# Performance work log

Hardware: AMD Instinct MI355X
Metric: run time of the kernel (lower is better)

The kernel has to match this reference:

```python
import jax, jax.numpy as jnp
import numpy as np
import math

D_MODEL = 1024
N_HEADS = 16
D_HEAD = D_MODEL // N_HEADS
LSR_RANK = 32
B, T = 4, 2048


def setup_inputs() -> dict:
    key = jax.random.key(0)
    ks = jax.random.split(key, 11)
    s = 1.0 / math.sqrt(D_MODEL)
    x = jax.random.normal(ks[0], (B, T, D_MODEL), dtype=jnp.float32)
    Wq = jax.random.uniform(ks[1], (D_MODEL, D_MODEL), minval=-s, maxval=s)
    bq = jax.random.uniform(ks[2], (D_MODEL,), minval=-s, maxval=s)
    Wk = jax.random.uniform(ks[3], (D_MODEL, D_MODEL), minval=-s, maxval=s)
    bk = jax.random.uniform(ks[4], (D_MODEL,), minval=-s, maxval=s)
    Wv = jax.random.uniform(ks[5], (D_MODEL, D_MODEL), minval=-s, maxval=s)
    bv = jax.random.uniform(ks[6], (D_MODEL,), minval=-s, maxval=s)
    Wo = jax.random.uniform(ks[7], (D_MODEL, D_MODEL), minval=-s, maxval=s)
    bo = jax.random.uniform(ks[8], (D_MODEL,), minval=-s, maxval=s)
    Wq_lsr = jax.random.normal(ks[9], (N_HEADS, D_HEAD, LSR_RANK)) / math.sqrt(D_HEAD)
    Wk_lsr = jax.random.normal(ks[10], (N_HEADS, D_HEAD, LSR_RANK)) / math.sqrt(D_HEAD)
    return {"x": x, "Wq": Wq, "bq": bq, "Wk": Wk, "bk": bk,
            "Wv": Wv, "bv": bv, "Wo": Wo, "bo": bo,
            "Wq_lsr": Wq_lsr, "Wk_lsr": Wk_lsr}


def reference(x, Wq, bq, Wk, bk, Wv, bv, Wo, bo, Wq_lsr, Wk_lsr):
    Bq, Tq, _ = x.shape
    # Linear projections (torch Linear: x @ W.T + b), split into heads -> (B,H,T,Dh)
    def split_heads(y):
        return y.reshape(Bq, Tq, N_HEADS, D_HEAD).transpose(0, 2, 1, 3)
    q = split_heads(x @ Wq.T + bq)
    k = split_heads(x @ Wk.T + bk)
    v = split_heads(x @ Wv.T + bv)
    # LSR: project q,k to rank-R per head
    q_lr = jnp.einsum('bhtd,hdr->bhtr', q, Wq_lsr)
    k_lr = jnp.einsum('bhtd,hdr->bhtr', k, Wk_lsr)
    scale = 1.0 / math.sqrt(max(LSR_RANK, 1))
    scores = jnp.einsum('bhir,bhjr->bhij', q_lr, k_lr) * scale  # (B,H,T,T)
    causal_mask = jnp.triu(jnp.ones((Tq, Tq), dtype=bool), k=1)
    scores = jnp.where(causal_mask, jnp.float32(-jnp.inf), scores)
    attn = jax.nn.softmax(scores, axis=-1)
    y = jnp.einsum('bhij,bhjd->bhid', attn, v)  # (B,H,T,Dh)
    y = y.transpose(0, 2, 1, 3).reshape(Bq, Tq, D_MODEL)
    return y @ Wo.T + bo
```

## Files before the change

### kernel.cpp

```cpp
#include <hip/hip_runtime.h>

#define B_  4
#define T_  2048
#define H_  16
#define DM_ 1024
#define DH_ 64
#define RK_ 32

using u16 = unsigned short;
using u32 = unsigned int;
typedef float  floatx4 __attribute__((ext_vector_type(4)));
typedef __bf16 bf16x8  __attribute__((ext_vector_type(8)));
typedef u16    u16x8   __attribute__((ext_vector_type(8)));
typedef u16    u16x4   __attribute__((ext_vector_type(4)));
typedef short  s16x4   __attribute__((ext_vector_type(4)));

#define MFMA16(a,b,c) __builtin_amdgcn_mfma_f32_16x16x32_bf16((a),(b),(c),0,0,0)
#define MFMA1K(a,b,c) __builtin_amdgcn_mfma_f32_16x16x16bf16_1k((a),(b),(c),0,0,0)

__device__ __forceinline__ u16 f2bf(float f) {
  unsigned u = __float_as_uint(f);
  u += 0x7fffu + ((u >> 16) & 1u);
  return (u16)(u >> 16);
}
__device__ __forceinline__ u32 pack_bf(float a, float b) {
  u32 ua = __float_as_uint(a); ua += 0x7fffu + ((ua >> 16) & 1u);
  u32 ub = __float_as_uint(b); ub += 0x7fffu + ((ub >> 16) & 1u);
  return __builtin_amdgcn_perm(ub, ua, 0x07060302u);
}
__device__ __forceinline__ u32 tpack(float a, float b) {
  return __builtin_amdgcn_perm(__float_as_uint(b), __float_as_uint(a), 0x07060302u);
}

__device__ __forceinline__ void async_copy16(const u16* g, const u16* lds_uniform_base) {
  __builtin_amdgcn_global_load_lds(
      (const __attribute__((address_space(1))) unsigned int*)(unsigned long long)g,
      (__attribute__((address_space(3))) unsigned int*)(unsigned int)(unsigned long long)lds_uniform_base,
      16, 0, 0);
}

__global__ __launch_bounds__(256) void cvt_x(const float* __restrict__ s,
                                             u16* __restrict__ d, int n4) {
  int i = blockIdx.x * 256 + threadIdx.x;
  if (i >= n4) return;
  float4 v = reinterpret_cast<const float4*>(s)[i];
  u16x4 o = { f2bf(v.x), f2bf(v.y), f2bf(v.z), f2bf(v.w) };
  reinterpret_cast<u16x4*>(d)[i] = o;
}

__global__ __launch_bounds__(256) void prep_w(const float* __restrict__ Wv,
                                              const float* __restrict__ Wo,
                                              const float* __restrict__ Wq,
                                              const float* __restrict__ bq,
                                              const float* __restrict__ Wql,
                                              const float* __restrict__ Wk,
                                              const float* __restrict__ bk,
                                              const float* __restrict__ Wkl,
                                              u16* __restrict__ Wcat,
                                              float* __restrict__ beffq,
                                              float* __restrict__ beffk) {
  const int tid = threadIdx.x;
  const int bid = blockIdx.x;
  __shared__ float lw[64];
  if (bid < 2048) {
    int i = bid * 256 + tid;
    int reg = i >> 18;
    const float* s = reg ? Wo : Wv;
    int j = i & 262143;
    float4 v = reinterpret_cast<const float4*>(s)[j];
    u16x4 o = { f2bf(v.x), f2bf(v.y), f2bf(v.z), f2bf(v.w) };
    reinterpret_cast<u16x4*>(Wcat)[(reg ? 524288 : 0) + j] = o;
    return;
  }
  const int sel = (bid >= 2560);
  const int hr = bid - (sel ? 2560 : 2048);
  const int h = hr >> 5, r = hr & 31;
  const float* W    = sel ? Wk : Wq;
  const float* bias = sel ? bk : bq;
  const float* lsr  = sel ? Wkl : Wql;
  const float fold  = sel ? 1.0f : 0.25506100790944405f;
  u16*   Weff = Wcat + (sel ? 1572864 : 1048576);
  float* beff = sel ? beffk : beffq;
  if (tid < 64) lw[tid] = lsr[(size_t)(h * 64 + tid) * 32 + r] * fold;
  __syncthreads();
  float a0 = 0.f, a1 = 0.f, a2 = 0.f, a3 = 0.f;
  for (int d = 0; d < 64; d++) {
    float l = lw[d];
    float4 wv = *reinterpret_cast<const float4*>(W + (size_t)(h * 64 + d) * 1024 + tid * 4);
    a0 += l * wv.x; a1 += l * wv.y; a2 += l * wv.z; a3 += l * wv.w;
  }
  u16x4 o = { f2bf(a0), f2bf(a1), f2bf(a2), f2bf(a3) };
  reinterpret_cast<u16x4*>(Weff)[(size_t)hr * 256 + tid] = o;
  if (tid == 0) {
    float s = 0.f;
    for (int d = 0; d < 64; d++) s += lw[d] * bias[h * 64 + d];
    beff[hr] = s;
  }
}

template <int MODE>
__global__ __launch_bounds__(256, 2) void gemm8(const u16* __restrict__ A,
                                                const u16* __restrict__ W,
                                                const float* __restrict__ b0,
                                                const float* __restrict__ b1,
                                                const float* __restrict__ b2,
                                                void* __restrict__ Cv,
                                                u16* __restrict__ qo,
                                                u16* __restrict__ ko,
                                                int ldc) {
  __shared__ __align__(16) u16 Al[2][8192];
  __shared__ __align__(16) u16 Bl[2][8192];
  const int tid  = threadIdx.x;
  const int lane = tid & 63;
  const int w    = tid >> 6;
  const int quad = lane >> 4;
  const int l16  = lane & 15;
  const int wm   = (w >> 1) << 6;
  const int wn   = (w & 1) << 6;

  const int bm = blockIdx.x << 7;
  const int bn = blockIdx.y << 7;

  const int sr = tid >> 3;
  const int sc = ((tid & 7) ^ (sr & 7)) * 8;
  const u16* Ag = A + (size_t)(bm + sr) * 1024 + sc;
  const u16* Wg = W + (size_t)(bn + sr) * 1024 + sc;

  auto stage = [&](int k0, int bsel) {
#pragma unroll
    for (int j = 0; j < 4; j++)
      async_copy16(Ag + (size_t)j * 32768 + k0, &Al[bsel][j * 2048 + w * 512]);
#pragma unroll
    for (int j = 0; j < 4; j++)
      async_copy16(Wg + (size_t)j * 32768 + k0, &Bl[bsel][j * 2048 + w * 512]);
  };

  int aoff[4], boff[4], sl[2];
#pragma unroll
  for (int mi = 0; mi < 4; mi++) aoff[mi] = (wm + mi * 16 + l16) * 64;
#pragma unroll
  for (int ni = 0; ni < 4; ni++) boff[ni] = (wn + ni * 16 + l16) * 64;
  sl[0] = ((0 + quad) ^ (l16 & 7)) * 8;
  sl[1] = ((4 + quad) ^ (l16 & 7)) * 8;

  floatx4 acc[4][4];
#pragma unroll
  for (int i = 0; i < 4; i++)
#pragma unroll
    for (int j = 0; j < 4; j++) acc[i][j] = (floatx4){0.f, 0.f, 0.f, 0.f};

  stage(0, 0);
  asm volatile("s_waitcnt vmcnt(0)" ::: "memory");
  __builtin_amdgcn_s_barrier();
  asm volatile("" ::: "memory");

  for (int i = 0; i < 16; i++) {
    if (i < 15) stage((i + 1) * 64, (i + 1) & 1);
    const u16* Ab = Al[i & 1];
    const u16* Bb = Bl[i & 1];
#pragma unroll
    for (int ks = 0; ks < 2; ks++) {
      bf16x8 af[4], bfr[4];
#pragma unroll
      for (int mi = 0; mi < 4; mi++)
        af[mi] = *reinterpret_cast<const bf16x8*>(Ab + aoff[mi] + sl[ks]);
#pragma unroll
      for (int ni = 0; ni < 4; ni++)
        bfr[ni] = *reinterpret_cast<const bf16x8*>(Bb + boff[ni] + sl[ks]);
      __builtin_amdgcn_s_setprio(1);
#pragma unroll
      for (int mi = 0; mi < 4; mi++)
#pragma unroll
        for (int ni = 0; ni < 4; ni++)
          acc[mi][ni] = MFMA16(af[mi], bfr[ni], acc[mi][ni]);
      __builtin_amdgcn_s_setprio(0);
    }
    if (i < 15) {
      asm volatile("s_waitcnt vmcnt(0)" ::: "memory");
      __builtin_amdgcn_s_barrier();
      asm volatile("" ::: "memory");
    }
  }

  if (MODE == 1) {
#pragma unroll
    for (int ni = 0; ni < 4; ni++) {
      int col = bn + wn + ni * 16 + l16;
      float bias = b0[col & 1023];
#pragma unroll
      for (int mi = 0; mi < 4; mi++)
#pragma unroll
        for (int r = 0; r < 4; r++) {
          int row = bm + wm + mi * 16 + quad * 4 + r;
          reinterpret_cast<float*>(Cv)[(size_t)row * ldc + col] = acc[mi][ni][r] + bias;
        }
    }
  } else {
    if (bn < 1024) {
#pragma unroll
      for (int ni = 0; ni < 4; ni++) {
        int col = bn + wn + ni * 16 + l16;
        float bias = b0[col];
#pragma unroll
        for (int mi = 0; mi < 4; mi++)
#pragma unroll
          for (int r = 0; r < 4; r++) {
            int row = bm + wm + mi * 16 + quad * 4 + r;
            reinterpret_cast<u16*>(Cv)[(size_t)row * 1024 + col] =
                f2bf(acc[mi][ni][r] + bias);
          }
      }
    } else {
      u16* outp = (bn < 1536) ? qo : ko;
      const float* bp = (bn < 1536) ? b1 : b2;
#pragma unroll
      for (int ni = 0; ni < 4; ni++) {
        int cc = (bn + wn + ni * 16 + l16) & 511;
        float bias = bp[cc];
        int hh = cc >> 5, rk = cc & 31;
#pragma unroll
        for (int mi = 0; mi < 4; mi++)
#pragma unroll
          for (int r = 0; r < 4; r++) {
            int row = bm + wm + mi * 16 + quad * 4 + r;
            size_t addr =
                ((size_t)((row >> 11) * 16 + hh) * 2048 + (row & 2047)) * 32 + rk;
            outp[addr] = f2bf(acc[mi][ni][r] + bias);
          }
      }
    }
  }
}

__global__ __launch_bounds__(256) void vtrans(const u16* __restrict__ V,
                                              u16* __restrict__ vt) {
  const int tb = blockIdx.x;
  const int bh = blockIdx.y;
  const int b = bh >> 4, h = bh & 15;
  __shared__ u16 Vl[64][72];
  const int tid = threadIdx.x;
#pragma unroll
  for (int it = 0; it < 2; it++) {
    int c = it * 256 + tid;
    int t = c >> 3, dc = (c & 7) * 8;
    u16x8 v = *reinterpret_cast<const u16x8*>(
        V + (size_t)(b * T_ + tb * 64 + t) * 1024 + h * 64 + dc);
    *reinterpret_cast<u16x8*>(&Vl[t][dc]) = v;
  }
  __syncthreads();
#pragma unroll
  for (int it = 0; it < 2; it++) {
    int c = it * 256 + tid;
    int d = c >> 3, tt = (c & 7) * 8;
    u16x8 o;
#pragma unroll
    for (int j = 0; j < 8; j++) o[j] = Vl[tt + j][d];
    *reinterpret_cast<u16x8*>(vt + ((size_t)bh * 64 + d) * T_ + tb * 64 + tt) = o;
  }
}

__global__ __launch_bounds__(256, 2) void attn(const u16* __restrict__ qlr,
                                               const u16* __restrict__ klr,
                                               const u16* __restrict__ vt,
                                               u16* __restrict__ yatt) {
  const int bh = blockIdx.x;
  const int b = bh >> 4, h = bh & 15;
  const int p = blockIdx.y;
  const int tid = threadIdx.x, lane = tid & 63, w = tid >> 6;
  const int quad = lane >> 4, l16 = lane & 15;

  __shared__ __align__(16) u16 Vt2[2][8192];
  __shared__ __align__(16) u16 Kt2[2][4096];

  const u16* qlr_bh = qlr + (size_t)bh * T_ * RK_;
  const u16* klr_bh = klr + (size_t)bh * T_ * RK_;
  const u16* vt_bh  = vt + (size_t)bh * 64 * T_;

  int voffN[8];
#pragma unroll
  for (int nt = 0; nt < 8; nt++)
    voffN[nt] = l16 * 128 + (((nt * 2 + (quad >> 1)) ^ l16) * 8) + (quad & 1) * 4;
  const int koff = (l16 >> 1) * 64 + ((((l16 & 1) * 4 + quad) ^ (l16 >> 1)) * 8);

  int soffV[4];
#pragma unroll
  for (int it = 0; it < 4; it++) {
    int L = it * 256 + tid;
    int d = L >> 4, s = L & 15;
    soffV[it] = d * T_ + ((s ^ (d & 15)) * 8);
  }
  int soffK[2];
#pragma unroll
  for (int it = 0; it < 2; it++) {
    int L = it * 256 + tid;
    int pr = L >> 3, s = L & 7;
    soffK[it] = pr * 64 + ((s ^ (pr & 7)) * 8);
  }
  const int wub = w * 512;

  const floatx4 fzero = {0.f, 0.f, 0.f, 0.f};
  const int thrq = w * 16 + l16;

  for (int run = 0; run < 2; run++) {
    const int j = run ? p : 15 - p;
    const int q0 = j << 7;
    const int nkt = j + 1;

    bf16x8 qf[2];
#pragma unroll
    for (int qg = 0; qg < 2; qg++)
      qf[qg] = *reinterpret_cast<const bf16x8*>(
          qlr_bh + (size_t)(q0 + qg * 64 + thrq) * 32 + quad * 8);

    auto stage = [&](int t, int bi) {
#pragma unroll
      for (int it = 0; it < 4; it++)
        async_copy16(vt_bh + t * 128 + soffV[it], &Vt2[bi][it * 2048 + wub]);
#pragma unroll
      for (int it = 0; it < 2; it++)
        async_copy16(klr_bh + t * 4096 + soffK[it], &Kt2[bi][it * 2048 + wub]);
    };

    stage(0, 0);
    asm volatile("s_waitcnt vmcnt(0)" ::: "memory");
    __builtin_amdgcn_s_barrier();
    asm volatile("" ::: "memory");

    floatx4 oacc[4][2];
#pragma unroll
    for (int i = 0; i < 4; i++)
#pragma unroll
      for (int jg = 0; jg < 2; jg++) oacc[i][jg] = fzero;
    float rs[2] = {0.f, 0.f};

    for (int i = 0; i < nkt; i++) {
      const bool last = (i == nkt - 1);
      if (!last) stage(i + 1, (i + 1) & 1);
      const u16* Vb = &Vt2[i & 1][0];
      const u16* Kb = &Kt2[i & 1][0];

      bf16x8 kf[8];
#pragma unroll
      for (int nt = 0; nt < 8; nt++)
        kf[nt] = *reinterpret_cast<const bf16x8*>(Kb + koff + nt * 512);

      uint2 pk[8][2];
      if (!last) {
#pragma unroll
        for (int qg = 0; qg < 2; qg++) {
          __builtin_amdgcn_s_setprio(1);
          floatx4 sv[8];
#pragma unroll
          for (int nt = 0; nt < 8; nt++) sv[nt] = MFMA16(kf[nt], qf[qg], fzero);
          __builtin_amdgcn_s_setprio(0);
#pragma unroll
          for (int nt = 0; nt < 8; nt++) {
            float p0 = __builtin_amdgcn_exp2f(sv[nt][0]);
            float p1 = __builtin_amdgcn_exp2f(sv[nt][1]);
            float p2 = __builtin_amdgcn_exp2f(sv[nt][2]);
            float p3 = __builtin_amdgcn_exp2f(sv[nt][3]);
            rs[qg] += (p0 + p1) + (p2 + p3);
            pk[nt][qg].x = tpack(p0, p1);
            pk[nt][qg].y = tpack(p2, p3);
          }
        }
      } else {
#pragma unroll
        for (int qg = 0; qg < 2; qg++) {
          const int thr = qg * 64 + thrq;
#pragma unroll
          for (int nt = 0; nt < 8; nt++) {
            floatx4 sv = MFMA16(kf[nt], qf[qg], fzero);
            const int keyl = nt * 16 + quad * 4;
            float pr[4];
#pragma unroll
            for (int r = 0; r < 4; r++) {
              float e = __builtin_amdgcn_exp2f(sv[r]);
              pr[r] = (keyl + r <= thr) ? e : 0.f;
            }
            rs[qg] += (pr[0] + pr[1]) + (pr[2] + pr[3]);
            pk[nt][qg].x = tpack(pr[0], pr[1]);
            pk[nt][qg].y = tpack(pr[2], pr[3]);
          }
        }
      }

      __builtin_amdgcn_s_setprio(1);
#pragma unroll
      for (int dt = 0; dt < 4; dt++)
#pragma unroll
        for (int nt = 0; nt < 8; nt++) {
          s16x4 vf = *reinterpret_cast<const s16x4*>(Vb + voffN[nt] + dt * 2048);
          oacc[dt][0] = MFMA1K(vf, __builtin_bit_cast(s16x4, pk[nt][0]), oacc[dt][0]);
          oacc[dt][1] = MFMA1K(vf, __builtin_bit_cast(s16x4, pk[nt][1]), oacc[dt][1]);
        }
      __builtin_amdgcn_s_setprio(0);

      asm volatile("s_waitcnt vmcnt(0)" ::: "memory");
      __builtin_amdgcn_s_barrier();
      asm volatile("" ::: "memory");
    }

#pragma unroll
    for (int qg = 0; qg < 2; qg++) {
      rs[qg] += __shfl_xor(rs[qg], 16);
      rs[qg] += __shfl_xor(rs[qg], 32);
    }
#pragma unroll
    for (int qg = 0; qg < 2; qg++) {
      float inv = 1.f / rs[qg];
      const int qrow = q0 + qg * 64 + thrq;
#pragma unroll
      for (int dt = 0; dt < 4; dt++) {
        uint2 ov = { pack_bf(oacc[dt][qg][0] * inv, oacc[dt][qg][1] * inv),
                     pack_bf(oacc[dt][qg][2] * inv, oacc[dt][qg][3] * inv) };
        *reinterpret_cast<uint2*>(
            yatt + (size_t)(b * T_ + qrow) * 1024 + h * 64 + dt * 16 + quad * 4) = ov;
      }
    }
  }
}

extern "C" void kernel_launch(void* const* d_in, const int* in_sizes, int n_in,
                              void* d_out, int out_size, void* d_ws, size_t ws_size,
                              hipStream_t stream) {
  const float* x   = (const float*)d_in[0];
  const float* Wq  = (const float*)d_in[1];
  const float* bq  = (const float*)d_in[2];
  const float* Wk  = (const float*)d_in[3];
  const float* bk  = (const float*)d_in[4];
  const float* Wv  = (const float*)d_in[5];
  const float* bv  = (const float*)d_in[6];
  const float* Wo  = (const float*)d_in[7];
  const float* bo  = (const float*)d_in[8];
  const float* Wql = (const float*)d_in[9];
  const float* Wkl = (const float*)d_in[10];
  float* out = (float*)d_out;

  char* ws = (char*)d_ws;
  u16*   xb    = (u16*)(ws);
  u16*   Wcat  = (u16*)(ws + 16777216);
  float* beffq = (float*)(ws + 23068672);
  float* beffk = (float*)(ws + 23072768);
  u16*   Vbuf  = (u16*)(ws + 25165824);
  u16*   qlr   = (u16*)(ws + 41943040);
  u16*   klr   = (u16*)(ws + 50331648);
  u16*   yatt  = (u16*)(ws + 58720256);
  u16*   vt    = xb;

  cvt_x<<<dim3(8192), 256, 0, stream>>>(x, xb, 2097152);
  prep_w<<<dim3(3072), 256, 0, stream>>>(Wv, Wo, Wq, bq, Wql, Wk, bk, Wkl,
                                         Wcat, beffq, beffk);
  gemm8<2><<<dim3(64, 16), 256, 0, stream>>>(xb, Wcat, bv, beffq, beffk,
                                             Vbuf, qlr, klr, 0);
  vtrans<<<dim3(32, 64), 256, 0, stream>>>(Vbuf, vt);
  attn<<<dim3(64, 8), 256, 0, stream>>>(qlr, klr, vt, yatt);
  gemm8<1><<<dim3(64, 8), 256, 0, stream>>>(yatt, Wcat + 2097152, bo, bo, bo,
                                            out, nullptr, nullptr, 1024);
}
```

Before: 234.5 us.

## Rewrite attention core to per-wave independent query tiles with register-prefetched K/V from global

Replaces the block-cooperative LDS double-buffered K/V staging with a scheme where each wave owns a 64-query tile and streams K and V fragments directly from global memory into registers, ping-ponging two register sets as a software prefetch. This removes LDS traffic and the per-tile block barriers, and the causal diagonal is handled by a dedicated masked tail. In exchange there is no K/V sharing between waves through LDS, so cache traffic rises. Load balance now depends on grid order, and the launch grid in the unseen host code must match the new indexing (31 - (blockIdx.y*4 + w)).

```diff
diff --git a/kernel.cpp b/kernel.cpp
--- a/kernel.cpp
+++ b/kernel.cpp
@@ -265,160 +265,146 @@
                                                u16* __restrict__ yatt) {
   const int bh = blockIdx.x;
   const int b = bh >> 4, h = bh & 15;
-  const int p = blockIdx.y;
   const int tid = threadIdx.x, lane = tid & 63, w = tid >> 6;
   const int quad = lane >> 4, l16 = lane & 15;
-
-  __shared__ __align__(16) u16 Vt2[2][8192];
-  __shared__ __align__(16) u16 Kt2[2][4096];
+  const int u = 31 - (blockIdx.y * 4 + w);
+  const int q0 = u * 64;
 
   const u16* qlr_bh = qlr + (size_t)bh * T_ * RK_;
   const u16* klr_bh = klr + (size_t)bh * T_ * RK_;
   const u16* vt_bh  = vt + (size_t)bh * 64 * T_;
 
-  int voffN[8];
-#pragma unroll
-  for (int nt = 0; nt < 8; nt++)
-    voffN[nt] = l16 * 128 + (((nt * 2 + (quad >> 1)) ^ l16) * 8) + (quad & 1) * 4;
-  const int koff = (l16 >> 1) * 64 + ((((l16 & 1) * 4 + quad) ^ (l16 >> 1)) * 8);
-
-  int soffV[4];
-#pragma unroll
-  for (int it = 0; it < 4; it++) {
-    int L = it * 256 + tid;
-    int d = L >> 4, s = L & 15;
-    soffV[it] = d * T_ + ((s ^ (d & 15)) * 8);
-  }
-  int soffK[2];
-#pragma unroll
-  for (int it = 0; it < 2; it++) {
-    int L = it * 256 + tid;
-    int pr = L >> 3, s = L & 7;
-    soffK[it] = pr * 64 + ((s ^ (pr & 7)) * 8);
-  }
-  const int wub = w * 512;
+  bf16x8 qf[4];
+#pragma unroll
+  for (int qg = 0; qg < 4; qg++)
+    qf[qg] = *reinterpret_cast<const bf16x8*>(
+        qlr_bh + (size_t)(q0 + qg * 16 + l16) * 32 + quad * 8);
+
+  const u16* kbase = klr_bh + (size_t)l16 * 32 + quad * 8;
+  const u16* vbase = vt_bh + (size_t)l16 * 2048 + quad * 4;
 
   const floatx4 fzero = {0.f, 0.f, 0.f, 0.f};
-  const int thrq = w * 16 + l16;
-
-  for (int run = 0; run < 2; run++) {
-    const int j = run ? p : 15 - p;
-    const int q0 = j << 7;
-    const int nkt = j + 1;
-
-    bf16x8 qf[2];
-#pragma unroll
-    for (int qg = 0; qg < 2; qg++)
-      qf[qg] = *reinterpret_cast<const bf16x8*>(
-          qlr_bh + (size_t)(q0 + qg * 64 + thrq) * 32 + quad * 8);
-
-    auto stage = [&](int t, int bi) {
-#pragma unroll
-      for (int it = 0; it < 4; it++)
-        async_copy16(vt_bh + t * 128 + soffV[it], &Vt2[bi][it * 2048 + wub]);
-#pragma unroll
-      for (int it = 0; it < 2; it++)
-        async_copy16(klr_bh + t * 4096 + soffK[it], &Kt2[bi][it * 2048 + wub]);
-    };
-
-    stage(0, 0);
-    asm volatile("s_waitcnt vmcnt(0)" ::: "memory");
-    __builtin_amdgcn_s_barrier();
-    asm volatile("" ::: "memory");
-
-    floatx4 oacc[4][2];
-#pragma unroll
-    for (int i = 0; i < 4; i++)
-#pragma unroll
-      for (int jg = 0; jg < 2; jg++) oacc[i][jg] = fzero;
-    float rs[2] = {0.f, 0.f};
-
-    for (int i = 0; i < nkt; i++) {
-      const bool last = (i == nkt - 1);
-      if (!last) stage(i + 1, (i + 1) & 1);
-      const u16* Vb = &Vt2[i & 1][0];
-      const u16* Kb = &Kt2[i & 1][0];
-
-      bf16x8 kf[8];
-#pragma unroll
-      for (int nt = 0; nt < 8; nt++)
-        kf[nt] = *reinterpret_cast<const bf16x8*>(Kb + koff + nt * 512);
-
-      uint2 pk[8][2];
-      if (!last) {
-#pragma unroll
-        for (int qg = 0; qg < 2; qg++) {
-          __builtin_amdgcn_s_setprio(1);
-          floatx4 sv[8];
-#pragma unroll
-          for (int nt = 0; nt < 8; nt++) sv[nt] = MFMA16(kf[nt], qf[qg], fzero);
-          __builtin_amdgcn_s_setprio(0);
-#pragma unroll
-          for (int nt = 0; nt < 8; nt++) {
-            float p0 = __builtin_amdgcn_exp2f(sv[nt][0]);
-            float p1 = __builtin_amdgcn_exp2f(sv[nt][1]);
-            float p2 = __builtin_amdgcn_exp2f(sv[nt][2]);
-            float p3 = __builtin_amdgcn_exp2f(sv[nt][3]);
-            rs[qg] += (p0 + p1) + (p2 + p3);
-            pk[nt][qg].x = tpack(p0, p1);
-            pk[nt][qg].y = tpack(p2, p3);
-          }
-        }
-      } else {
-#pragma unroll
-        for (int qg = 0; qg < 2; qg++) {
-          const int thr = qg * 64 + thrq;
-#pragma unroll
-          for (int nt = 0; nt < 8; nt++) {
-            floatx4 sv = MFMA16(kf[nt], qf[qg], fzero);
-            const int keyl = nt * 16 + quad * 4;
-            float pr[4];
-#pragma unroll
-            for (int r = 0; r < 4; r++) {
-              float e = __builtin_amdgcn_exp2f(sv[r]);
-              pr[r] = (keyl + r <= thr) ? e : 0.f;
-            }
-            rs[qg] += (pr[0] + pr[1]) + (pr[2] + pr[3]);
-            pk[nt][qg].x = tpack(pr[0], pr[1]);
-            pk[nt][qg].y = tpack(pr[2], pr[3]);
-          }
-        }
-      }
-
-      __builtin_amdgcn_s_setprio(1);
-#pragma unroll
-      for (int dt = 0; dt < 4; dt++)
-#pragma unroll
-        for (int nt = 0; nt < 8; nt++) {
-          s16x4 vf = *reinterpret_cast<const s16x4*>(Vb + voffN[nt] + dt * 2048);
-          oacc[dt][0] = MFMA1K(vf, __builtin_bit_cast(s16x4, pk[nt][0]), oacc[dt][0]);
-          oacc[dt][1] = MFMA1K(vf, __builtin_bit_cast(s16x4, pk[nt][1]), oacc[dt][1]);
-        }
-      __builtin_amdgcn_s_setprio(0);
-
-      asm volatile("s_waitcnt vmcnt(0)" ::: "memory");
-      __builtin_amdgcn_s_barrier();
-      asm volatile("" ::: "memory");
+  floatx4 oacc[4][4];
+#pragma unroll
+  for (int i = 0; i < 4; i++)
+#pragma unroll
+    for (int j = 0; j < 4; j++) oacc[i][j] = fzero;
+  float rs[4] = {0.f, 0.f, 0.f, 0.f};
+
+  bf16x8 kfA[2], kfB[2];
+  s16x4  vfA[4][2], vfB[4][2];
+
+#define LOADK(dst, ck)                                                          \
+  {                                                                             \
+    _Pragma("unroll") for (int sub = 0; sub < 2; sub++)                         \
+      dst[sub] = *reinterpret_cast<const bf16x8*>(                              \
+          kbase + (size_t)((ck) * 32 + sub * 16) * 32);                         \
+  }
+#define LOADV(dst, ck)                                                          \
+  {                                                                             \
+    _Pragma("unroll") for (int dt = 0; dt < 4; dt++)                            \
+      _Pragma("unroll") for (int sub = 0; sub < 2; sub++)                       \
+        dst[dt][sub] = *reinterpret_cast<const s16x4*>(                         \
+            vbase + (size_t)dt * 32768 + (ck) * 32 + sub * 16);                 \
+  }
+#define COMPUTE_FULL(kf, vf)                                                    \
+  {                                                                             \
+    uint2 pk[2][4];                                                             \
+    __builtin_amdgcn_s_setprio(1);                                              \
+    _Pragma("unroll") for (int sub = 0; sub < 2; sub++)                         \
+      _Pragma("unroll") for (int qg = 0; qg < 4; qg++) {                        \
+        floatx4 sv = MFMA16(kf[sub], qf[qg], fzero);                            \
+        float p0 = __builtin_amdgcn_exp2f(sv[0]);                               \
+        float p1 = __builtin_amdgcn_exp2f(sv[1]);                               \
+        float p2 = __builtin_amdgcn_exp2f(sv[2]);                               \
+        float p3 = __builtin_amdgcn_exp2f(sv[3]);                               \
+        rs[qg] += (p0 + p1) + (p2 + p3);                                        \
+        pk[sub][qg].x = tpack(p0, p1);                                          \
+        pk[sub][qg].y = tpack(p2, p3);                                          \
+      }                                                                         \
+    _Pragma("unroll") for (int dt = 0; dt < 4; dt++)                            \
+      _Pragma("unroll") for (int sub = 0; sub < 2; sub++)                       \
+        _Pragma("unroll") for (int qg = 0; qg < 4; qg++)                        \
+          oacc[dt][qg] =                                                        \
+              MFMA1K(vf[dt][sub], __builtin_bit_cast(s16x4, pk[sub][qg]),       \
+                     oacc[dt][qg]);                                             \
+    __builtin_amdgcn_s_setprio(0);                                              \
+  }
+#define SM_DIAG(kf_s, qg)                                                       \
+  {                                                                             \
+    floatx4 sv = MFMA16(kf_s, qf[qg], fzero);                                   \
+    const int keyl = quad * 4;                                                  \
+    float pr0 = (keyl + 0 <= l16) ? __builtin_amdgcn_exp2f(sv[0]) : 0.f;        \
+    float pr1 = (keyl + 1 <= l16) ? __builtin_amdgcn_exp2f(sv[1]) : 0.f;        \
+    float pr2 = (keyl + 2 <= l16) ? __builtin_amdgcn_exp2f(sv[2]) : 0.f;        \
+    float pr3 = (keyl + 3 <= l16) ? __builtin_amdgcn_exp2f(sv[3]) : 0.f;        \
+    rs[qg] += (pr0 + pr1) + (pr2 + pr3);                                        \
+    pkm.x = tpack(pr0, pr1);                                                    \
+    pkm.y = tpack(pr2, pr3);                                                    \
+  }
+#define SM_FULL(kf_s, qg)                                                       \
+  {                                                                             \
+    floatx4 sv = MFMA16(kf_s, qf[qg], fzero);                                   \
+    float p0 = __builtin_amdgcn_exp2f(sv[0]);                                   \
+    float p1 = __builtin_amdgcn_exp2f(sv[1]);                                   \
+    float p2 = __builtin_amdgcn_exp2f(sv[2]);                                   \
+    float p3 = __builtin_amdgcn_exp2f(sv[3]);                                   \
+    rs[qg] += (p0 + p1) + (p2 + p3);                                            \
+    pkm.x = tpack(p0, p1);                                                      \
+    pkm.y = tpack(p2, p3);                                                      \
+  }
+#define PV_ONE(vf, sub, qg)                                                     \
+  _Pragma("unroll") for (int dt = 0; dt < 4; dt++)                              \
+    oacc[dt][qg] = MFMA1K(vf[dt][sub], __builtin_bit_cast(s16x4, pkm),          \
+                          oacc[dt][qg]);
+
+  LOADK(kfA, 0); LOADV(vfA, 0);
+  LOADK(kfB, 1); LOADV(vfB, 1);
+
+  for (int t = 0; t < u; t++) {
+    COMPUTE_FULL(kfA, vfA);
+    LOADK(kfA, 2 * t + 2); LOADV(vfA, 2 * t + 2);
+    COMPUTE_FULL(kfB, vfB);
+    LOADK(kfB, 2 * t + 3); LOADV(vfB, 2 * t + 3);
+  }
+
+  {
+    uint2 pkm;
+    SM_DIAG(kfA[0], 0); PV_ONE(vfA, 0, 0);
+    SM_FULL(kfA[0], 1); PV_ONE(vfA, 0, 1);
+    SM_FULL(kfA[0], 2); PV_ONE(vfA, 0, 2);
+    SM_FULL(kfA[0], 3); PV_ONE(vfA, 0, 3);
+    SM_DIAG(kfA[1], 1); PV_ONE(vfA, 1, 1);
+    SM_FULL(kfA[1], 2); PV_ONE(vfA, 1, 2);
+    SM_FULL(kfA[1], 3); PV_ONE(vfA, 1, 3);
+    SM_DIAG(kfB[0], 2); PV_ONE(vfB, 0, 2);
+    SM_FULL(kfB[0], 3); PV_ONE(vfB, 0, 3);
+    SM_DIAG(kfB[1], 3); PV_ONE(vfB, 1, 3);
+  }
+
+#pragma unroll
+  for (int qg = 0; qg < 4; qg++) {
+    rs[qg] += __shfl_xor(rs[qg], 16);
+    rs[qg] += __shfl_xor(rs[qg], 32);
+  }
+#pragma unroll
+  for (int qg = 0; qg < 4; qg++) {
+    float inv = 1.f / rs[qg];
+    const int qrow = q0 + qg * 16 + l16;
+#pragma unroll
+    for (int dt = 0; dt < 4; dt++) {
+      uint2 ov = { pack_bf(oacc[dt][qg][0] * inv, oacc[dt][qg][1] * inv),
+                   pack_bf(oacc[dt][qg][2] * inv, oacc[dt][qg][3] * inv) };
+      *reinterpret_cast<uint2*>(
+          yatt + (size_t)(b * T_ + qrow) * 1024 + h * 64 + dt * 16 + quad * 4) = ov;
     }
-
-#pragma unroll
-    for (int qg = 0; qg < 2; qg++) {
-      rs[qg] += __shfl_xor(rs[qg], 16);
-      rs[qg] += __shfl_xor(rs[qg], 32);
-    }
-#pragma unroll
-    for (int qg = 0; qg < 2; qg++) {
-      float inv = 1.f / rs[qg];
-      const int qrow = q0 + qg * 64 + thrq;
-#pragma unroll
-      for (int dt = 0; dt < 4; dt++) {
-        uint2 ov = { pack_bf(oacc[dt][qg][0] * inv, oacc[dt][qg][1] * inv),
-                     pack_bf(oacc[dt][qg][2] * inv, oacc[dt][qg][3] * inv) };
-        *reinterpret_cast<uint2*>(
-            yatt + (size_t)(b * T_ + qrow) * 1024 + h * 64 + dt * 16 + quad * 4) = ov;
-      }
-    }
-  }
+  }
+#undef LOADK
+#undef LOADV
+#undef COMPUTE_FULL
+#undef SM_DIAG
+#undef SM_FULL
+#undef PV_ONE
 }
 
 extern "C" void kernel_launch(void* const* d_in, const int* in_sizes, int n_in,
```

Result: slower. 286.1 us (+22.0%).
